# Kernel optimization log

Measured on AMD Instinct MI355X. Metric: run time of the kernel, lower is better.

## Reference

```python
import jax, jax.numpy as jnp
import numpy as np

V, E, H, L = 100000, 128, 512, 9
B, T = 64, 512


def setup_inputs() -> dict:
    key = jax.random.key(0)
    ks = jax.random.split(key, 8)
    text = jax.random.randint(ks[0], (B, T), 0, V, dtype=jnp.int32)
    labels = jax.random.randint(ks[1], (B, T), 0, L, dtype=jnp.int32)
    embed = jax.random.normal(ks[2], (V, E), jnp.float32) * 0.02
    Wx = jax.random.normal(ks[3], (E, 4 * H), jnp.float32) * (1.0 / np.sqrt(E))
    Wh = jax.random.normal(ks[4], (H, 4 * H), jnp.float32) * (1.0 / np.sqrt(H))
    # Keras LSTM default: zero bias with unit forget-gate bias (gate order i,f,c,o)
    b = jnp.zeros((4 * H,), jnp.float32).at[H:2 * H].set(1.0)
    Wd = jax.random.normal(ks[5], (H, L), jnp.float32) * (1.0 / np.sqrt(H))
    bd = jnp.zeros((L,), jnp.float32)
    trans = jax.random.uniform(ks[6], (L, L), jnp.float32)
    return dict(text=text, labels=labels, embed=embed, Wx=Wx, Wh=Wh, b=b,
                Wd=Wd, bd=bd, trans=trans)


def _lstm(x, Wx, Wh, b):
    # x: [B,T,E] -> h: [B,T,H]; Keras gate order i,f,c,o
    Bx, Tx, _ = x.shape
    Hh = Wh.shape[0]
    xg = jnp.einsum('bte,eg->btg', x, Wx) + b  # precompute input projections [B,T,4H]

    def step(carry, g_t):
        h, c = carry
        g = g_t + h @ Wh
        i, f, cg, o = jnp.split(g, 4, axis=-1)
        c = jax.nn.sigmoid(f) * c + jax.nn.sigmoid(i) * jnp.tanh(cg)
        h = jax.nn.sigmoid(o) * jnp.tanh(c)
        return (h, c), h

    init = (jnp.zeros((Bx, Hh), x.dtype), jnp.zeros((Bx, Hh), x.dtype))
    _, hs = jax.lax.scan(step, init, jnp.moveaxis(xg, 1, 0))
    return jnp.moveaxis(hs, 0, 1)


def _crf_log_likelihood(logits, labels, lens, trans):
    # tfa.text.crf_log_likelihood: score(seq) - log_norm (forward algorithm)
    Bl, Tl, Ll = logits.shape
    t_idx = jnp.arange(Tl)
    mask = t_idx[None, :] < lens[:, None]  # [B,T]
    unary = jnp.take_along_axis(logits, labels[..., None], axis=2)[..., 0]
    unary = jnp.where(mask, unary, 0.0).sum(-1)
    binary = trans[labels[:, :-1], labels[:, 1:]]
    bmask = t_idx[1:][None, :] < lens[:, None]  # transition t->t+1 counts iff t+1 < len
    binary = jnp.where(bmask, binary, 0.0).sum(-1)
    score = unary + binary

    def step(alpha, xs):
        lg, t = xs  # lg: [B,L]
        new = jax.scipy.special.logsumexp(alpha[:, :, None] + trans[None], axis=1) + lg
        alpha = jnp.where((t < lens)[:, None], new, alpha)
        return alpha, None

    alpha0 = logits[:, 0]
    xs = (jnp.moveaxis(logits[:, 1:], 1, 0), jnp.arange(1, Tl))
    alpha, _ = jax.lax.scan(step, alpha0, xs)
    log_norm = jax.scipy.special.logsumexp(alpha, axis=-1)
    return score - log_norm


def reference(text, labels, embed, Wx, Wh, b, Wd, bd, trans):
    lens = jnp.sum((text != 0).astype(jnp.int32), axis=-1)
    x = embed[text]                      # [B,T,E] (dropout inactive at inference)
    h = _lstm(x, Wx, Wh, b)              # [B,T,H]
    logits = h @ Wd + bd                 # [B,T,L]
    ll = _crf_log_likelihood(logits, labels, lens, trans)  # [B]
    return logits, lens, ll
```

## Files before the change

kernel.cpp:

```cpp
#include <hip/hip_runtime.h>
#include <hip/hip_bf16.h>

#define V_SZ 100000
#define E_SZ 128
#define H_SZ 512
#define L_SZ 9
#define B_SZ 64
#define T_SZ 512
#define G4   (4*H_SZ)

#define LOGITS_N (B_SZ*T_SZ*L_SZ)
#define HS_BYTES ((size_t)B_SZ*T_SZ*H_SZ*2)
#define SENT32 0x7FC07FC0u
#define SENT64 0x7FC07FC07FC07FC0ull

typedef short bf16x8 __attribute__((ext_vector_type(8)));
typedef float f32x4  __attribute__((ext_vector_type(4)));

static __device__ __forceinline__ unsigned short f2bf(float x){
  unsigned int u = __builtin_bit_cast(unsigned int, x);
  unsigned int r = (u + 0x7fffu + ((u >> 16) & 1u)) >> 16;
  return (unsigned short)r;
}
static __device__ __forceinline__ float bf2f(unsigned short b){
  unsigned int u = ((unsigned int)b) << 16;
  return __builtin_bit_cast(float, u);
}
static __device__ __forceinline__ float sig_f(float x){
  return 1.f / (1.f + __expf(-x));
}
static __device__ __forceinline__ float tanh_f(float x){
  float a = fabsf(x);
  float e = __expf(-2.f * a);
  float t = (1.f - e) / (1.f + e);
  return copysignf(t, x);
}

__global__ void k_reset(unsigned long long* __restrict__ hs64){
  const long n = HS_BYTES / 8;
  for (long i = (long)blockIdx.x*256 + threadIdx.x; i < n; i += (long)gridDim.x*256)
    __hip_atomic_store(&hs64[i], SENT64, __ATOMIC_RELAXED, __HIP_MEMORY_SCOPE_AGENT);
}

__global__ void k_lens(const int* __restrict__ text, float* __restrict__ out_lens){
  int b = blockIdx.x;
  int c = 0;
  for (int t = threadIdx.x; t < T_SZ; t += 256)
    c += (text[b*T_SZ + t] != 0);
  for (int off = 32; off; off >>= 1) c += __shfl_down(c, off, 64);
  __shared__ int sred[4];
  int w = threadIdx.x >> 6;
  if ((threadIdx.x & 63) == 0) sred[w] = c;
  __syncthreads();
  if (threadIdx.x == 0)
    out_lens[b] = (float)(sred[0] + sred[1] + sred[2] + sred[3]);
}

__global__ __launch_bounds__(256, 1)
void k_lstm(const int* __restrict__ text, const float* __restrict__ embed,
            const float* __restrict__ Wx, const float* __restrict__ Wh,
            const float* __restrict__ bias, unsigned short* __restrict__ hs)
{
  const int p    = blockIdx.x & 3;
  const int j    = blockIdx.x >> 2;
  const int n0   = j * 16;
  const int tid  = threadIdx.x;
  const int w    = tid >> 6;
  const int lane = tid & 63;
  const int q    = lane >> 4;
  const int l16  = lane & 15;
  const int gate = l16 & 3;
  const int cq   = l16 >> 2;

  __shared__ unsigned short h_lds[2][16*512];
  __shared__ unsigned short x_lds[2][16*128];

  const int hcol = n0 + w*4 + cq;
  const int gcol = gate*H_SZ + hcol;
  bf16x8 Whf[16];
#pragma unroll
  for (int kk = 0; kk < 16; ++kk){
    bf16x8 v;
#pragma unroll
    for (int jj = 0; jj < 8; ++jj)
      v[jj] = (short)f2bf(Wh[(long)(kk*32 + q*8 + jj)*G4 + gcol]);
    Whf[kk] = v;
  }
  bf16x8 Wxf[4];
#pragma unroll
  for (int kk = 0; kk < 4; ++kk){
    bf16x8 v;
#pragma unroll
    for (int jj = 0; jj < 8; ++jj)
      v[jj] = (short)f2bf(Wx[(long)(kk*32 + q*8 + jj)*G4 + gcol]);
    Wxf[kk] = v;
  }
  const float biasv = bias[gcol];

  float cs[4] = {0.f, 0.f, 0.f, 0.f};
  const bool isPub = (l16 == 0);

  unsigned short* ppub[4];
#pragma unroll
  for (int rg = 0; rg < 4; ++rg)
    ppub[rg] = hs + ((long)(p*16 + q*4 + rg)*T_SZ)*H_SZ + n0 + w*4;

  const int xr = tid >> 4;
  const int c8 = (tid & 15) * 8;
  const int cb = c8 * 2;
  unsigned short* xdst[2];
#pragma unroll
  for (int pb = 0; pb < 2; ++pb)
    xdst[pb] = (unsigned short*)((char*)x_lds[pb] + xr*256 + (cb ^ (xr << 4)));
  const int* tokp = text + (p*16 + xr)*T_SZ;

  {
    int tok = tokp[0];
    const float4 xv0 = *(const float4*)(embed + (long)tok*E_SZ + c8);
    const float4 xv1 = *(const float4*)(embed + (long)tok*E_SZ + c8 + 4);
    unsigned short* pp = xdst[0];
    pp[0] = f2bf(xv0.x); pp[1] = f2bf(xv0.y); pp[2] = f2bf(xv0.z); pp[3] = f2bf(xv0.w);
    pp[4] = f2bf(xv1.x); pp[5] = f2bf(xv1.y); pp[6] = f2bf(xv1.z); pp[7] = f2bf(xv1.w);
  }

  for (int t = 0; t < T_SZ; ++t){
    const int par = t & 1;

    if (t > 0){
      unsigned long long v[8];
      int it = 0; bool ok;
      do {
        ok = true;
#pragma unroll
        for (int c = 0; c < 8; ++c){
          int chunk = tid + 256*c;
          int hr    = chunk >> 7;
          int k4    = chunk & 127;
          v[c] = __hip_atomic_load(
              (const unsigned long long*)(hs + ((long)(p*16 + hr)*T_SZ + (t-1))*H_SZ + k4*4),
              __ATOMIC_RELAXED, __HIP_MEMORY_SCOPE_AGENT);
        }
#pragma unroll
        for (int c = 0; c < 8; ++c)
          ok = ok && ((unsigned int)v[c] != SENT32);
      } while (!ok && ++it < (1 << 20));
#pragma unroll
      for (int c = 0; c < 8; ++c){
        int chunk = tid + 256*c;
        int hr    = chunk >> 7;
        int k4    = chunk & 127;
        *(unsigned long long*)((char*)h_lds[par] + hr*1024 + ((k4*8) ^ (hr << 4))) = v[c];
      }
    }
    __syncthreads();

    float4 xv0, xv1; bool havex = (t + 1 < T_SZ);
    if (havex){
      int tok = tokp[t + 1];
      xv0 = *(const float4*)(embed + (long)tok*E_SZ + c8);
      xv1 = *(const float4*)(embed + (long)tok*E_SZ + c8 + 4);
    }

    f32x4 acc0 = {biasv, biasv, biasv, biasv};
    f32x4 acc1 = {0.f, 0.f, 0.f, 0.f};
#pragma unroll
    for (int kk = 0; kk < 4; ++kk){
      bf16x8 a = *(const bf16x8*)((const char*)x_lds[par] + l16*256 + ((kk*64 + q*16) ^ (l16 << 4)));
      if (kk & 1) acc1 = __builtin_amdgcn_mfma_f32_16x16x32_bf16(a, Wxf[kk], acc1, 0, 0, 0);
      else        acc0 = __builtin_amdgcn_mfma_f32_16x16x32_bf16(a, Wxf[kk], acc0, 0, 0, 0);
    }
    if (t > 0){
#pragma unroll
      for (int kk = 0; kk < 16; ++kk){
        bf16x8 a = *(const bf16x8*)((const char*)h_lds[par] + l16*1024 + ((kk*64 + q*16) ^ (l16 << 4)));
        if (kk & 1) acc1 = __builtin_amdgcn_mfma_f32_16x16x32_bf16(a, Whf[kk], acc1, 0, 0, 0);
        else        acc0 = __builtin_amdgcn_mfma_f32_16x16x32_bf16(a, Whf[kk], acc0, 0, 0, 0);
      }
    }

#pragma unroll
    for (int rg = 0; rg < 4; ++rg){
      float v  = acc0[rg] + acc1[rg];
      float x1 = __shfl_xor(v, 1, 64);
      float x2 = __shfl_xor(v, 2, 64);
      float x3 = __shfl_xor(v, 3, 64);
      float gi = (gate==0)? v : (gate==1)? x1 : (gate==2)? x2 : x3;
      float gf = (gate==1)? v : (gate==0)? x1 : (gate==3)? x2 : x3;
      float gc = (gate==2)? v : (gate==3)? x1 : (gate==0)? x2 : x3;
      float go = (gate==3)? v : (gate==2)? x1 : (gate==1)? x2 : x3;
      cs[rg] = sig_f(gf)*cs[rg] + sig_f(gi)*tanh_f(gc);
      float hv = sig_f(go)*tanh_f(cs[rg]);
      unsigned int hb = (unsigned int)f2bf(hv);
      unsigned int pr  = (unsigned int)__shfl_xor((int)hb, 4, 64);
      unsigned int pk  = hb | (pr << 16);
      unsigned int pk2 = (unsigned int)__shfl_xor((int)pk, 8, 64);
      unsigned long long p8 = (unsigned long long)pk
                            | ((unsigned long long)pk2 << 32);
      if (isPub)
        __hip_atomic_store((unsigned long long*)ppub[rg], p8,
                           __ATOMIC_RELAXED, __HIP_MEMORY_SCOPE_AGENT);
    }
#pragma unroll
    for (int rg = 0; rg < 4; ++rg) ppub[rg] += H_SZ;

    if (havex){
      unsigned short* pp = xdst[par ^ 1];
      pp[0] = f2bf(xv0.x); pp[1] = f2bf(xv0.y); pp[2] = f2bf(xv0.z); pp[3] = f2bf(xv0.w);
      pp[4] = f2bf(xv1.x); pp[5] = f2bf(xv1.y); pp[6] = f2bf(xv1.z); pp[7] = f2bf(xv1.w);
    }
  }
}

__global__ void k_logits(const unsigned short* __restrict__ hs,
                         const float* __restrict__ Wd, const float* __restrict__ bd,
                         float* __restrict__ out)
{
  __shared__ float wd_s[H_SZ*L_SZ];
  __shared__ float bd_s[L_SZ];
  for (int i = threadIdx.x; i < H_SZ*L_SZ; i += 128) wd_s[i] = Wd[i];
  if (threadIdx.x < L_SZ) bd_s[threadIdx.x] = bd[threadIdx.x];
  __syncthreads();

  long row = (long)blockIdx.x*128 + threadIdx.x;
  const unsigned short* hp = hs + row*H_SZ;
  float acc[9];
#pragma unroll
  for (int jj = 0; jj < 9; ++jj) acc[jj] = 0.f;
  for (int k = 0; k < H_SZ; k += 8){
    uint4 v = *(const uint4*)(hp + k);
    const unsigned short* u = (const unsigned short*)&v;
#pragma unroll
    for (int l = 0; l < 8; ++l){
      float hf = bf2f(u[l]);
#pragma unroll
      for (int jj = 0; jj < 9; ++jj)
        acc[jj] = fmaf(hf, wd_s[(k + l)*L_SZ + jj], acc[jj]);
    }
  }
  float* op = out + row*L_SZ;
#pragma unroll
  for (int jj = 0; jj < 9; ++jj) op[jj] = acc[jj] + bd_s[jj];
}

__global__ void k_crf(const float* __restrict__ logits, const int* __restrict__ labels,
                      const float* __restrict__ trans, const float* __restrict__ lensf,
                      float* __restrict__ out_ll)
{
  int b = blockIdx.x;
  int lane = threadIdx.x;
  int len = (int)lensf[b];
  const float* lg  = logits + (long)b*T_SZ*L_SZ;
  const int*   lab = labels + b*T_SZ;

  float s = 0.f;
  for (int t = lane; t < T_SZ; t += 64){
    if (t < len){
      s += lg[t*L_SZ + lab[t]];
      if (t >= 1) s += trans[lab[t-1]*L_SZ + lab[t]];
    }
  }
  for (int off = 32; off; off >>= 1) s += __shfl_down(s, off, 64);

  float tr[9];
#pragma unroll
  for (int i = 0; i < 9; ++i) tr[i] = (lane < 9) ? trans[i*L_SZ + lane] : 0.f;
  float alpha = (lane < 9) ? lg[lane] : -1e30f;

  for (int t = 1; t < T_SZ; ++t){
    float tmp[9];
#pragma unroll
    for (int i = 0; i < 9; ++i){
      float ai = __shfl(alpha, i, 64);
      tmp[i] = ai + tr[i];
    }
    float m0 = fmaxf(fmaxf(tmp[0], tmp[1]), tmp[2]);
    float m1 = fmaxf(fmaxf(tmp[3], tmp[4]), tmp[5]);
    float m2 = fmaxf(fmaxf(tmp[6], tmp[7]), tmp[8]);
    float m  = fmaxf(fmaxf(m0, m1), m2);
    float e = 0.f;
#pragma unroll
    for (int i = 0; i < 9; ++i) e += __expf(tmp[i] - m);
    float lgv = (lane < 9) ? lg[t*L_SZ + lane] : 0.f;
    float nv = m + __logf(e) + lgv;
    if (t < len && lane < 9) alpha = nv;
  }

  float mm = (lane < 9) ? alpha : -1e30f;
  for (int off = 8; off; off >>= 1) mm = fmaxf(mm, __shfl_down(mm, off, 64));
  mm = __shfl(mm, 0, 64);
  float ee = (lane < 9) ? __expf(alpha - mm) : 0.f;
  for (int off = 8; off; off >>= 1) ee += __shfl_down(ee, off, 64);
  if (lane == 0) out_ll[b] = s - (mm + __logf(ee));
}

extern "C" void kernel_launch(void* const* d_in, const int* in_sizes, int n_in,
                              void* d_out, int out_size, void* d_ws, size_t ws_size,
                              hipStream_t stream)
{
  const int*   text   = (const int*)  d_in[0];
  const int*   labels = (const int*)  d_in[1];
  const float* embed  = (const float*)d_in[2];
  const float* Wx     = (const float*)d_in[3];
  const float* Wh     = (const float*)d_in[4];
  const float* bias   = (const float*)d_in[5];
  const float* Wd     = (const float*)d_in[6];
  const float* bd     = (const float*)d_in[7];
  const float* trans  = (const float*)d_in[8];

  float* out        = (float*)d_out;
  float* out_logits = out;
  float* out_lens   = out + LOGITS_N;
  float* out_ll     = out + LOGITS_N + B_SZ;

  unsigned short* hs = (unsigned short*)d_ws;

  k_reset <<<2048, 256, 0, stream>>>((unsigned long long*)hs);
  k_lens  <<<B_SZ, 256, 0, stream>>>(text, out_lens);
  k_lstm  <<<128, 256, 0, stream>>>(text, embed, Wx, Wh, bias, hs);
  k_logits<<<256, 128, 0, stream>>>(hs, Wd, bd, out_logits);
  k_crf   <<<B_SZ, 64, 0, stream>>>(out_logits, labels, trans, out_lens, out_ll);
}
```

Before: 1.676 ms.

## Halve LSTM block count with 32 hidden columns per block and double-buffered polling

Each persistent LSTM block now computes 32 hidden columns instead of 16, so the grid shrinks from 128 to 64 blocks. Each block then has fewer peers to wait for, and per-step cross-block sync traffic is cut in half. The spin loop that polls for the previous step's hidden state now overlaps the next load with the sentinel check, and __syncthreads is replaced by an explicit lgkmcnt wait plus s_barrier. The cost is doubled register pressure for the weight fragments (32 Whf and 8 Wxf bf16x8 vectors), which risks spills, and twice the MFMA and activation work per block on the serial critical path.

```diff
diff --git a/kernel.cpp b/kernel.cpp
--- a/kernel.cpp
+++ b/kernel.cpp
@@ -63,7 +63,7 @@
 {
   const int p    = blockIdx.x & 3;
   const int j    = blockIdx.x >> 2;
-  const int n0   = j * 16;
+  const int n0   = j * 32;
   const int tid  = threadIdx.x;
   const int w    = tid >> 6;
   const int lane = tid & 63;
@@ -75,35 +75,44 @@
   __shared__ unsigned short h_lds[2][16*512];
   __shared__ unsigned short x_lds[2][16*128];
 
-  const int hcol = n0 + w*4 + cq;
-  const int gcol = gate*H_SZ + hcol;
-  bf16x8 Whf[16];
+  const int wc    = n0 + w*8;
+  const int gcol0 = gate*H_SZ + wc + cq;
+  const int gcol1 = gcol0 + 4;
+  bf16x8 Whf0[16], Whf1[16];
 #pragma unroll
   for (int kk = 0; kk < 16; ++kk){
-    bf16x8 v;
-#pragma unroll
-    for (int jj = 0; jj < 8; ++jj)
-      v[jj] = (short)f2bf(Wh[(long)(kk*32 + q*8 + jj)*G4 + gcol]);
-    Whf[kk] = v;
-  }
-  bf16x8 Wxf[4];
+    bf16x8 v0, v1;
+#pragma unroll
+    for (int jj = 0; jj < 8; ++jj){
+      const float* wr = Wh + (long)(kk*32 + q*8 + jj)*G4;
+      v0[jj] = (short)f2bf(wr[gcol0]);
+      v1[jj] = (short)f2bf(wr[gcol1]);
+    }
+    Whf0[kk] = v0; Whf1[kk] = v1;
+  }
+  bf16x8 Wxf0[4], Wxf1[4];
 #pragma unroll
   for (int kk = 0; kk < 4; ++kk){
-    bf16x8 v;
-#pragma unroll
-    for (int jj = 0; jj < 8; ++jj)
-      v[jj] = (short)f2bf(Wx[(long)(kk*32 + q*8 + jj)*G4 + gcol]);
-    Wxf[kk] = v;
-  }
-  const float biasv = bias[gcol];
-
-  float cs[4] = {0.f, 0.f, 0.f, 0.f};
+    bf16x8 v0, v1;
+#pragma unroll
+    for (int jj = 0; jj < 8; ++jj){
+      const float* wr = Wx + (long)(kk*32 + q*8 + jj)*G4;
+      v0[jj] = (short)f2bf(wr[gcol0]);
+      v1[jj] = (short)f2bf(wr[gcol1]);
+    }
+    Wxf0[kk] = v0; Wxf1[kk] = v1;
+  }
+  const float biasv0 = bias[gcol0];
+  const float biasv1 = bias[gcol1];
+
+  float cs0[4] = {0.f,0.f,0.f,0.f};
+  float cs1[4] = {0.f,0.f,0.f,0.f};
   const bool isPub = (l16 == 0);
 
   unsigned short* ppub[4];
 #pragma unroll
   for (int rg = 0; rg < 4; ++rg)
-    ppub[rg] = hs + ((long)(p*16 + q*4 + rg)*T_SZ)*H_SZ + n0 + w*4;
+    ppub[rg] = hs + ((long)(p*16 + q*4 + rg)*T_SZ)*H_SZ + wc;
 
   const int xr = tid >> 4;
   const int c8 = (tid & 15) * 8;
@@ -127,32 +136,55 @@
     const int par = t & 1;
 
     if (t > 0){
-      unsigned long long v[8];
-      int it = 0; bool ok;
-      do {
-        ok = true;
+      const unsigned short* hbase = hs + (long)(t-1)*H_SZ + (long)(p*16)*T_SZ*H_SZ;
+      unsigned long long va[8], vb[8];
+      auto loadA = [&](unsigned long long* v){
 #pragma unroll
         for (int c = 0; c < 8; ++c){
           int chunk = tid + 256*c;
           int hr    = chunk >> 7;
           int k4    = chunk & 127;
           v[c] = __hip_atomic_load(
-              (const unsigned long long*)(hs + ((long)(p*16 + hr)*T_SZ + (t-1))*H_SZ + k4*4),
+              (const unsigned long long*)(hbase + (long)hr*T_SZ*H_SZ + k4*4),
               __ATOMIC_RELAXED, __HIP_MEMORY_SCOPE_AGENT);
         }
+      };
+      auto okA = [&](const unsigned long long* v){
+        bool ok = true;
 #pragma unroll
         for (int c = 0; c < 8; ++c)
           ok = ok && ((unsigned int)v[c] != SENT32);
-      } while (!ok && ++it < (1 << 20));
+        return ok;
+      };
+      loadA(va);
+      bool useA = true; int it = 0;
+      for (;;){
+        if (useA){
+          loadA(vb);
+          if (okA(va)) break;
+        } else {
+          loadA(va);
+          if (okA(vb)){
+#pragma unroll
+            for (int c = 0; c < 8; ++c) va[c] = vb[c];
+            break;
+          }
+        }
+        useA = !useA;
+        if (++it > (1 << 20)) break;
+      }
 #pragma unroll
       for (int c = 0; c < 8; ++c){
         int chunk = tid + 256*c;
         int hr    = chunk >> 7;
         int k4    = chunk & 127;
-        *(unsigned long long*)((char*)h_lds[par] + hr*1024 + ((k4*8) ^ (hr << 4))) = v[c];
-      }
-    }
-    __syncthreads();
+        *(unsigned long long*)((char*)h_lds[par] + hr*1024 + ((k4*8) ^ (hr << 4))) = va[c];
+      }
+    }
+    asm volatile("s_waitcnt lgkmcnt(0)" ::: "memory");
+    __builtin_amdgcn_sched_barrier(0);
+    __builtin_amdgcn_s_barrier();
+    __builtin_amdgcn_sched_barrier(0);
 
     float4 xv0, xv1; bool havex = (t + 1 < T_SZ);
     if (havex){
@@ -161,44 +193,79 @@
       xv1 = *(const float4*)(embed + (long)tok*E_SZ + c8 + 4);
     }
 
-    f32x4 acc0 = {biasv, biasv, biasv, biasv};
-    f32x4 acc1 = {0.f, 0.f, 0.f, 0.f};
+    f32x4 a00 = {biasv0, biasv0, biasv0, biasv0};
+    f32x4 a01 = {0.f, 0.f, 0.f, 0.f};
+    f32x4 a10 = {biasv1, biasv1, biasv1, biasv1};
+    f32x4 a11 = {0.f, 0.f, 0.f, 0.f};
 #pragma unroll
     for (int kk = 0; kk < 4; ++kk){
       bf16x8 a = *(const bf16x8*)((const char*)x_lds[par] + l16*256 + ((kk*64 + q*16) ^ (l16 << 4)));
-      if (kk & 1) acc1 = __builtin_amdgcn_mfma_f32_16x16x32_bf16(a, Wxf[kk], acc1, 0, 0, 0);
-      else        acc0 = __builtin_amdgcn_mfma_f32_16x16x32_bf16(a, Wxf[kk], acc0, 0, 0, 0);
+      if (kk & 1){
+        a01 = __builtin_amdgcn_mfma_f32_16x16x32_bf16(a, Wxf0[kk], a01, 0, 0, 0);
+        a11 = __builtin_amdgcn_mfma_f32_16x16x32_bf16(a, Wxf1[kk], a11, 0, 0, 0);
+      } else {
+        a00 = __builtin_amdgcn_mfma_f32_16x16x32_bf16(a, Wxf0[kk], a00, 0, 0, 0);
+        a10 = __builtin_amdgcn_mfma_f32_16x16x32_bf16(a, Wxf1[kk], a10, 0, 0, 0);
+      }
     }
     if (t > 0){
 #pragma unroll
       for (int kk = 0; kk < 16; ++kk){
         bf16x8 a = *(const bf16x8*)((const char*)h_lds[par] + l16*1024 + ((kk*64 + q*16) ^ (l16 << 4)));
-        if (kk & 1) acc1 = __builtin_amdgcn_mfma_f32_16x16x32_bf16(a, Whf[kk], acc1, 0, 0, 0);
-        else        acc0 = __builtin_amdgcn_mfma_f32_16x16x32_bf16(a, Whf[kk], acc0, 0, 0, 0);
+        if (kk & 1){
+          a01 = __builtin_amdgcn_mfma_f32_16x16x32_bf16(a, Whf0[kk], a01, 0, 0, 0);
+          a11 = __builtin_amdgcn_mfma_f32_16x16x32_bf16(a, Whf1[kk], a11, 0, 0, 0);
+        } else {
+          a00 = __builtin_amdgcn_mfma_f32_16x16x32_bf16(a, Whf0[kk], a00, 0, 0, 0);
+          a10 = __builtin_amdgcn_mfma_f32_16x16x32_bf16(a, Whf1[kk], a10, 0, 0, 0);
+        }
       }
     }
 
 #pragma unroll
     for (int rg = 0; rg < 4; ++rg){
-      float v  = acc0[rg] + acc1[rg];
-      float x1 = __shfl_xor(v, 1, 64);
-      float x2 = __shfl_xor(v, 2, 64);
-      float x3 = __shfl_xor(v, 3, 64);
-      float gi = (gate==0)? v : (gate==1)? x1 : (gate==2)? x2 : x3;
-      float gf = (gate==1)? v : (gate==0)? x1 : (gate==3)? x2 : x3;
-      float gc = (gate==2)? v : (gate==3)? x1 : (gate==0)? x2 : x3;
-      float go = (gate==3)? v : (gate==2)? x1 : (gate==1)? x2 : x3;
-      cs[rg] = sig_f(gf)*cs[rg] + sig_f(gi)*tanh_f(gc);
-      float hv = sig_f(go)*tanh_f(cs[rg]);
-      unsigned int hb = (unsigned int)f2bf(hv);
-      unsigned int pr  = (unsigned int)__shfl_xor((int)hb, 4, 64);
-      unsigned int pk  = hb | (pr << 16);
-      unsigned int pk2 = (unsigned int)__shfl_xor((int)pk, 8, 64);
-      unsigned long long p8 = (unsigned long long)pk
-                            | ((unsigned long long)pk2 << 32);
-      if (isPub)
-        __hip_atomic_store((unsigned long long*)ppub[rg], p8,
-                           __ATOMIC_RELAXED, __HIP_MEMORY_SCOPE_AGENT);
+      {
+        float v  = a00[rg] + a01[rg];
+        float x1 = __shfl_xor(v, 1, 64);
+        float x2 = __shfl_xor(v, 2, 64);
+        float x3 = __shfl_xor(v, 3, 64);
+        float gi = (gate==0)? v : (gate==1)? x1 : (gate==2)? x2 : x3;
+        float gf = (gate==1)? v : (gate==0)? x1 : (gate==3)? x2 : x3;
+        float gc = (gate==2)? v : (gate==3)? x1 : (gate==0)? x2 : x3;
+        float go = (gate==3)? v : (gate==2)? x1 : (gate==1)? x2 : x3;
+        cs0[rg] = sig_f(gf)*cs0[rg] + sig_f(gi)*tanh_f(gc);
+        float hv = sig_f(go)*tanh_f(cs0[rg]);
+        unsigned int hb = (unsigned int)f2bf(hv);
+        unsigned int pr  = (unsigned int)__shfl_xor((int)hb, 4, 64);
+        unsigned int pk  = hb | (pr << 16);
+        unsigned int pk2 = (unsigned int)__shfl_xor((int)pk, 8, 64);
+        unsigned long long p8 = (unsigned long long)pk
+                              | ((unsigned long long)pk2 << 32);
+        if (isPub)
+          __hip_atomic_store((unsigned long long*)ppub[rg], p8,
+                             __ATOMIC_RELAXED, __HIP_MEMORY_SCOPE_AGENT);
+      }
+      {
+        float v  = a10[rg] + a11[rg];
+        float x1 = __shfl_xor(v, 1, 64);
+        float x2 = __shfl_xor(v, 2, 64);
+        float x3 = __shfl_xor(v, 3, 64);
+        float gi = (gate==0)? v : (gate==1)? x1 : (gate==2)? x2 : x3;
+        float gf = (gate==1)? v : (gate==0)? x1 : (gate==3)? x2 : x3;
+        float gc = (gate==2)? v : (gate==3)? x1 : (gate==0)? x2 : x3;
+        float go = (gate==3)? v : (gate==2)? x1 : (gate==1)? x2 : x3;
+        cs1[rg] = sig_f(gf)*cs1[rg] + sig_f(gi)*tanh_f(gc);
+        float hv = sig_f(go)*tanh_f(cs1[rg]);
+        unsigned int hb = (unsigned int)f2bf(hv);
+        unsigned int pr  = (unsigned int)__shfl_xor((int)hb, 4, 64);
+        unsigned int pk  = hb | (pr << 16);
+        unsigned int pk2 = (unsigned int)__shfl_xor((int)pk, 8, 64);
+        unsigned long long p8 = (unsigned long long)pk
+                              | ((unsigned long long)pk2 << 32);
+        if (isPub)
+          __hip_atomic_store((unsigned long long*)(ppub[rg] + 4), p8,
+                             __ATOMIC_RELAXED, __HIP_MEMORY_SCOPE_AGENT);
+      }
     }
 #pragma unroll
     for (int rg = 0; rg < 4; ++rg) ppub[rg] += H_SZ;
@@ -316,7 +383,7 @@
 
   k_reset <<<2048, 256, 0, stream>>>((unsigned long long*)hs);
   k_lens  <<<B_SZ, 256, 0, stream>>>(text, out_lens);
-  k_lstm  <<<128, 256, 0, stream>>>(text, embed, Wx, Wh, bias, hs);
+  k_lstm  <<<64, 256, 0, stream>>>(text, embed, Wx, Wh, bias, hs);
   k_logits<<<256, 128, 0, stream>>>(hs, Wd, bd, out_logits);
   k_crf   <<<B_SZ, 64, 0, stream>>>(out_logits, labels, trans, out_lens, out_ll);
 }
```

Measured after the change: 2.840 ms. 1.69x slower.

## Split LSTM into single-wave blocks loading h directly into registers

Applied to the files above, without the earlier changes.

The persistent LSTM kernel goes from 128 blocks of 4 waves to 1024 single-wave blocks. Each block handles 8 batch rows and 4 hidden columns, so the MFMA M dimension is half padding. Each wave polls the previous h step straight from global memory into registers and builds MFMA operands without LDS or __syncthreads. This removes the LDS staging and block barrier from the serial per-step path. In exchange it wastes half the MFMA rows, adds far more polling traffic, and needs all 1024 blocks co-resident for the spin-wait handshake to avoid deadlock.

```diff
diff --git a/kernel.cpp b/kernel.cpp
--- a/kernel.cpp
+++ b/kernel.cpp
@@ -16,6 +16,7 @@
 
 typedef short bf16x8 __attribute__((ext_vector_type(8)));
 typedef float f32x4  __attribute__((ext_vector_type(4)));
+typedef unsigned long long u64x2 __attribute__((ext_vector_type(2)));
 
 static __device__ __forceinline__ unsigned short f2bf(float x){
   unsigned int u = __builtin_bit_cast(unsigned int, x);
@@ -56,27 +57,22 @@
     out_lens[b] = (float)(sred[0] + sred[1] + sred[2] + sred[3]);
 }
 
-__global__ __launch_bounds__(256, 1)
+__global__ __launch_bounds__(64, 1)
 void k_lstm(const int* __restrict__ text, const float* __restrict__ embed,
             const float* __restrict__ Wx, const float* __restrict__ Wh,
             const float* __restrict__ bias, unsigned short* __restrict__ hs)
 {
-  const int p    = blockIdx.x & 3;
-  const int j    = blockIdx.x >> 2;
-  const int n0   = j * 16;
-  const int tid  = threadIdx.x;
-  const int w    = tid >> 6;
-  const int lane = tid & 63;
+  const int bid  = blockIdx.x;
+  const int g    = bid & 7;
+  const int wv   = bid >> 3;
+  const int wcb  = wv * 4;
+  const int lane = threadIdx.x;
   const int q    = lane >> 4;
   const int l16  = lane & 15;
   const int gate = l16 & 3;
   const int cq   = l16 >> 2;
 
-  __shared__ unsigned short h_lds[2][16*512];
-  __shared__ unsigned short x_lds[2][16*128];
-
-  const int hcol = n0 + w*4 + cq;
-  const int gcol = gate*H_SZ + hcol;
+  const int gcol = gate*H_SZ + wcb + cq;
   bf16x8 Whf[16];
 #pragma unroll
   for (int kk = 0; kk < 16; ++kk){
@@ -98,81 +94,89 @@
   const float biasv = bias[gcol];
 
   float cs[4] = {0.f, 0.f, 0.f, 0.f};
-  const bool isPub = (l16 == 0);
-
-  unsigned short* ppub[4];
+  const bool isPub = (l16 == 0) && (q < 2);
+
+  unsigned long long* ppub[4];
 #pragma unroll
   for (int rg = 0; rg < 4; ++rg)
-    ppub[rg] = hs + ((long)(p*16 + q*4 + rg)*T_SZ)*H_SZ + n0 + w*4;
-
-  const int xr = tid >> 4;
-  const int c8 = (tid & 15) * 8;
-  const int cb = c8 * 2;
-  unsigned short* xdst[2];
-#pragma unroll
-  for (int pb = 0; pb < 2; ++pb)
-    xdst[pb] = (unsigned short*)((char*)x_lds[pb] + xr*256 + (cb ^ (xr << 4)));
-  const int* tokp = text + (p*16 + xr)*T_SZ;
-
-  {
+    ppub[rg] = (unsigned long long*)(hs + ((long)(g*8 + q*4 + rg)*T_SZ)*H_SZ + wcb);
+
+  const unsigned long long* hb = (const unsigned long long*)hs
+      + (long)(g*8 + l16)*(T_SZ*H_SZ/4) + q*2;
+
+  const int* tokp = text + (g*8 + (l16 & 7))*T_SZ;
+
+  float4 xa[4], xb[4];
+  bf16x8 xf[4];
+#pragma unroll
+  for (int kk = 0; kk < 4; ++kk) xf[kk] = (bf16x8){0,0,0,0,0,0,0,0};
+  if (l16 < 8){
     int tok = tokp[0];
-    const float4 xv0 = *(const float4*)(embed + (long)tok*E_SZ + c8);
-    const float4 xv1 = *(const float4*)(embed + (long)tok*E_SZ + c8 + 4);
-    unsigned short* pp = xdst[0];
-    pp[0] = f2bf(xv0.x); pp[1] = f2bf(xv0.y); pp[2] = f2bf(xv0.z); pp[3] = f2bf(xv0.w);
-    pp[4] = f2bf(xv1.x); pp[5] = f2bf(xv1.y); pp[6] = f2bf(xv1.z); pp[7] = f2bf(xv1.w);
-  }
+    const float* er = embed + (long)tok*E_SZ + q*8;
+#pragma unroll
+    for (int kk = 0; kk < 4; ++kk){
+      xa[kk] = *(const float4*)(er + kk*32);
+      xb[kk] = *(const float4*)(er + kk*32 + 4);
+    }
+#pragma unroll
+    for (int kk = 0; kk < 4; ++kk){
+      bf16x8 v;
+      v[0] = (short)f2bf(xa[kk].x); v[1] = (short)f2bf(xa[kk].y);
+      v[2] = (short)f2bf(xa[kk].z); v[3] = (short)f2bf(xa[kk].w);
+      v[4] = (short)f2bf(xb[kk].x); v[5] = (short)f2bf(xb[kk].y);
+      v[6] = (short)f2bf(xb[kk].z); v[7] = (short)f2bf(xb[kk].w);
+      xf[kk] = v;
+    }
+  }
+
+  unsigned long long h0[16], h1[16];
+#pragma unroll
+  for (int kk = 0; kk < 16; ++kk){ h0[kk] = 0ull; h1[kk] = 0ull; }
 
   for (int t = 0; t < T_SZ; ++t){
-    const int par = t & 1;
-
     if (t > 0){
-      unsigned long long v[8];
       int it = 0; bool ok;
       do {
         ok = true;
-#pragma unroll
-        for (int c = 0; c < 8; ++c){
-          int chunk = tid + 256*c;
-          int hr    = chunk >> 7;
-          int k4    = chunk & 127;
-          v[c] = __hip_atomic_load(
-              (const unsigned long long*)(hs + ((long)(p*16 + hr)*T_SZ + (t-1))*H_SZ + k4*4),
-              __ATOMIC_RELAXED, __HIP_MEMORY_SCOPE_AGENT);
+        if (l16 < 8){
+#pragma unroll
+          for (int kk = 0; kk < 16; ++kk){
+            h0[kk] = __hip_atomic_load(hb + kk*8,     __ATOMIC_RELAXED,
+                                       __HIP_MEMORY_SCOPE_AGENT);
+            h1[kk] = __hip_atomic_load(hb + kk*8 + 1, __ATOMIC_RELAXED,
+                                       __HIP_MEMORY_SCOPE_AGENT);
+          }
+#pragma unroll
+          for (int kk = 0; kk < 16; ++kk)
+            ok = ok && ((unsigned int)h0[kk] != SENT32)
+                    && ((unsigned int)h1[kk] != SENT32);
         }
-#pragma unroll
-        for (int c = 0; c < 8; ++c)
-          ok = ok && ((unsigned int)v[c] != SENT32);
-      } while (!ok && ++it < (1 << 20));
-#pragma unroll
-      for (int c = 0; c < 8; ++c){
-        int chunk = tid + 256*c;
-        int hr    = chunk >> 7;
-        int k4    = chunk & 127;
-        *(unsigned long long*)((char*)h_lds[par] + hr*1024 + ((k4*8) ^ (hr << 4))) = v[c];
-      }
-    }
-    __syncthreads();
-
-    float4 xv0, xv1; bool havex = (t + 1 < T_SZ);
+      } while (!__all(ok) && ++it < (1 << 20));
+      hb += H_SZ/4;
+    }
+
+    const bool havex = (t + 1 < T_SZ) && (l16 < 8);
     if (havex){
       int tok = tokp[t + 1];
-      xv0 = *(const float4*)(embed + (long)tok*E_SZ + c8);
-      xv1 = *(const float4*)(embed + (long)tok*E_SZ + c8 + 4);
+      const float* er = embed + (long)tok*E_SZ + q*8;
+#pragma unroll
+      for (int kk = 0; kk < 4; ++kk){
+        xa[kk] = *(const float4*)(er + kk*32);
+        xb[kk] = *(const float4*)(er + kk*32 + 4);
+      }
     }
 
     f32x4 acc0 = {biasv, biasv, biasv, biasv};
     f32x4 acc1 = {0.f, 0.f, 0.f, 0.f};
 #pragma unroll
     for (int kk = 0; kk < 4; ++kk){
-      bf16x8 a = *(const bf16x8*)((const char*)x_lds[par] + l16*256 + ((kk*64 + q*16) ^ (l16 << 4)));
-      if (kk & 1) acc1 = __builtin_amdgcn_mfma_f32_16x16x32_bf16(a, Wxf[kk], acc1, 0, 0, 0);
-      else        acc0 = __builtin_amdgcn_mfma_f32_16x16x32_bf16(a, Wxf[kk], acc0, 0, 0, 0);
+      if (kk & 1) acc1 = __builtin_amdgcn_mfma_f32_16x16x32_bf16(xf[kk], Wxf[kk], acc1, 0, 0, 0);
+      else        acc0 = __builtin_amdgcn_mfma_f32_16x16x32_bf16(xf[kk], Wxf[kk], acc0, 0, 0, 0);
     }
     if (t > 0){
 #pragma unroll
       for (int kk = 0; kk < 16; ++kk){
-        bf16x8 a = *(const bf16x8*)((const char*)h_lds[par] + l16*1024 + ((kk*64 + q*16) ^ (l16 << 4)));
+        bf16x8 a = __builtin_bit_cast(bf16x8, (u64x2){h0[kk], h1[kk]});
         if (kk & 1) acc1 = __builtin_amdgcn_mfma_f32_16x16x32_bf16(a, Whf[kk], acc1, 0, 0, 0);
         else        acc0 = __builtin_amdgcn_mfma_f32_16x16x32_bf16(a, Whf[kk], acc0, 0, 0, 0);
       }
@@ -190,23 +194,29 @@
       float go = (gate==3)? v : (gate==2)? x1 : (gate==1)? x2 : x3;
       cs[rg] = sig_f(gf)*cs[rg] + sig_f(gi)*tanh_f(gc);
       float hv = sig_f(go)*tanh_f(cs[rg]);
-      unsigned int hb = (unsigned int)f2bf(hv);
-      unsigned int pr  = (unsigned int)__shfl_xor((int)hb, 4, 64);
-      unsigned int pk  = hb | (pr << 16);
+      unsigned int hb2 = (unsigned int)f2bf(hv);
+      unsigned int pr  = (unsigned int)__shfl_xor((int)hb2, 4, 64);
+      unsigned int pk  = hb2 | (pr << 16);
       unsigned int pk2 = (unsigned int)__shfl_xor((int)pk, 8, 64);
       unsigned long long p8 = (unsigned long long)pk
                             | ((unsigned long long)pk2 << 32);
       if (isPub)
-        __hip_atomic_store((unsigned long long*)ppub[rg], p8,
+        __hip_atomic_store(ppub[rg], p8,
                            __ATOMIC_RELAXED, __HIP_MEMORY_SCOPE_AGENT);
     }
 #pragma unroll
-    for (int rg = 0; rg < 4; ++rg) ppub[rg] += H_SZ;
+    for (int rg = 0; rg < 4; ++rg) ppub[rg] += H_SZ/4;
 
     if (havex){
-      unsigned short* pp = xdst[par ^ 1];
-      pp[0] = f2bf(xv0.x); pp[1] = f2bf(xv0.y); pp[2] = f2bf(xv0.z); pp[3] = f2bf(xv0.w);
-      pp[4] = f2bf(xv1.x); pp[5] = f2bf(xv1.y); pp[6] = f2bf(xv1.z); pp[7] = f2bf(xv1.w);
+#pragma unroll
+      for (int kk = 0; kk < 4; ++kk){
+        bf16x8 v;
+        v[0] = (short)f2bf(xa[kk].x); v[1] = (short)f2bf(xa[kk].y);
+        v[2] = (short)f2bf(xa[kk].z); v[3] = (short)f2bf(xa[kk].w);
+        v[4] = (short)f2bf(xb[kk].x); v[5] = (short)f2bf(xb[kk].y);
+        v[6] = (short)f2bf(xb[kk].z); v[7] = (short)f2bf(xb[kk].w);
+        xf[kk] = v;
+      }
     }
   }
 }
@@ -316,7 +326,7 @@
 
   k_reset <<<2048, 256, 0, stream>>>((unsigned long long*)hs);
   k_lens  <<<B_SZ, 256, 0, stream>>>(text, out_lens);
-  k_lstm  <<<128, 256, 0, stream>>>(text, embed, Wx, Wh, bias, hs);
+  k_lstm  <<<1024, 64, 0, stream>>>(text, embed, Wx, Wh, bias, hs);
   k_logits<<<256, 128, 0, stream>>>(hs, Wd, bd, out_logits);
   k_crf   <<<B_SZ, 64, 0, stream>>>(out_logits, labels, trans, out_lens, out_ll);
 }
```

Result: slower. 6.387 ms (+281.2%).
